# Optimization experiments

Hardware: AMD Instinct MI355X
Metric: run time of the kernel (lower is better)

Reference implementation:

```python
import jax, jax.numpy as jnp
import numpy as np

B, S, D, F, E, K = 2, 2048, 1024, 4096, 8, 2


def setup_inputs() -> dict:
    key = jax.random.key(0)
    ks = jax.random.split(key, 6)
    s = 0.02  # init scale
    return {
        "x": jax.random.normal(ks[0], (B, S, D), dtype=jnp.float32),
        "Wr": jax.random.normal(ks[1], (D, E), dtype=jnp.float32) * s,
        "br": jnp.zeros((E,), dtype=jnp.float32),
        "W1": jax.random.normal(ks[2], (E, D, F), dtype=jnp.float32) * s,
        "b1": jnp.zeros((E, F), dtype=jnp.float32),
        "W2": jax.random.normal(ks[3], (E, F, D), dtype=jnp.float32) * s,
        "b2": jnp.zeros((E, D), dtype=jnp.float32),
        "top_k": K,
    }


def reference(x, Wr, br, W1, b1, W2, b2, top_k):
    b, s, d = x.shape
    e = Wr.shape[1]
    xt = x.reshape(-1, d)                              # [T, D], T = b*s
    logits = xt @ Wr + br                              # [T, E]
    probs = jax.nn.softmax(logits, axis=-1)            # [T, E] router probabilities
    topw, topi = jax.lax.top_k(probs, top_k)           # [T, K] each
    # combine weight per (token, expert): weight if expert in token's top-k else 0
    cw = jnp.sum(jax.nn.one_hot(topi, e, dtype=x.dtype) * topw[..., None], axis=1)  # [T, E]
    # dense grouped FFN: every expert over every token, then weighted combine
    h = jax.nn.relu(jnp.einsum('td,edf->tef', xt, W1) + b1)   # [T, E, F]
    y = jnp.einsum('tef,efd->ted', h, W2) + b2                # [T, E, D]
    out = jnp.einsum('te,ted->td', cw, y).reshape(b, s, d)    # [B, S, D]
    return out, probs.reshape(b, s, e)
```

## Files before the change

kernel.cpp:

```cpp
#include <hip/hip_runtime.h>
#include <hip/hip_bf16.h>


#define T_TOK 4096
#define D_DIM 1024
#define F_DIM 4096
#define E_NUM 8
#define CAP_ROWS 9216
#define N_TILES (CAP_ROWS/128)

typedef __attribute__((ext_vector_type(8))) short short8v;
typedef __attribute__((ext_vector_type(8))) unsigned short ushort8v;
typedef __attribute__((ext_vector_type(4))) float f32x4;

static __device__ __forceinline__ unsigned short f2bf(float f){
  union { float f; unsigned u; } v; v.f = f;
  unsigned r = (v.u + 0x7fffu + ((v.u >> 16) & 1u)) >> 16;
  return (unsigned short)r;
}
static __device__ __forceinline__ float bf2f(unsigned short s){
  union { unsigned u; float f; } v; v.u = ((unsigned)s) << 16;
  return v.f;
}

static __device__ __forceinline__ void gload16(const void* g, void* l) {
  __builtin_amdgcn_global_load_lds(
      (const __attribute__((address_space(1))) unsigned int*)g,
      (__attribute__((address_space(3))) unsigned int*)l, 16, 0, 0);
}

__global__ __launch_bounds__(256) void k_init(int* counts, int* cursor,
                                              int* rows_token, float* rows_w){
  const int gid = blockIdx.x * 256 + threadIdx.x;
  if (gid < E_NUM) counts[gid] = 0;
  else if (gid < 2*E_NUM) cursor[gid - E_NUM] = 0;
  if (gid < CAP_ROWS) { rows_token[gid] = 0; rows_w[gid] = 0.f; }
}

__global__ __launch_bounds__(256) void k_router(
    const float* __restrict__ x, const float* __restrict__ Wr,
    const float* __restrict__ br, float* __restrict__ probs_out,
    int* __restrict__ topi, float* __restrict__ topw, int* __restrict__ counts,
    unsigned short* __restrict__ xbf)
{
  const int lane = threadIdx.x & 63;
  const int t = blockIdx.x * 4 + (threadIdx.x >> 6);
  float xv[16];
  #pragma unroll
  for (int i = 0; i < 16; ++i) xv[i] = x[(size_t)t*D_DIM + i*64 + lane];
  #pragma unroll
  for (int i = 0; i < 16; ++i) xbf[(size_t)t*D_DIM + i*64 + lane] = f2bf(xv[i]);
  float pe[E_NUM];
  #pragma unroll
  for (int e = 0; e < E_NUM; ++e) {
    float p = 0.f;
    #pragma unroll
    for (int i = 0; i < 16; ++i) p += xv[i] * Wr[(i*64 + lane)*E_NUM + e];
    #pragma unroll
    for (int off = 32; off >= 1; off >>= 1) p += __shfl_xor(p, off);
    pe[e] = p + br[e];
  }
  float m = pe[0];
  #pragma unroll
  for (int e = 1; e < E_NUM; ++e) m = fmaxf(m, pe[e]);
  float s = 0.f;
  #pragma unroll
  for (int e = 0; e < E_NUM; ++e) { pe[e] = expf(pe[e] - m); s += pe[e]; }
  const float inv = 1.f / s;
  int e1 = 0; float v1 = pe[0];
  #pragma unroll
  for (int e = 1; e < E_NUM; ++e) if (pe[e] > v1) { v1 = pe[e]; e1 = e; }
  int e2 = (e1 == 0) ? 1 : 0; float v2 = pe[e2];
  #pragma unroll
  for (int e = 0; e < E_NUM; ++e) if (e != e1 && pe[e] > v2) { v2 = pe[e]; e2 = e; }
  if (lane == 0) {
    #pragma unroll
    for (int e = 0; e < E_NUM; ++e) probs_out[(size_t)t*E_NUM + e] = pe[e] * inv;
    topi[t*2+0] = e1; topw[t*2+0] = v1 * inv;
    topi[t*2+1] = e2; topw[t*2+1] = v2 * inv;
    atomicAdd(&counts[e1], 1);
    atomicAdd(&counts[e2], 1);
  }
}

__global__ __launch_bounds__(256) void k_scan(
    const int* __restrict__ counts, int* __restrict__ pbase,
    int* __restrict__ tile_e)
{
  __shared__ int base_s[E_NUM + 1];
  const int tid = threadIdx.x;
  if (tid == 0) {
    int base = 0;
    #pragma unroll
    for (int e = 0; e < E_NUM; ++e) {
      base_s[e] = base;
      base += ((counts[e] + 127) >> 7) << 7;
    }
    base_s[E_NUM] = base;
  }
  __syncthreads();
  if (tid <= E_NUM) pbase[tid] = base_s[tid];
  if (tid < N_TILES) {
    const int r0 = tid << 7;
    int e = -1;
    #pragma unroll
    for (int k = 0; k < E_NUM; ++k)
      if (r0 >= base_s[k] && r0 < base_s[k+1]) e = k;
    tile_e[tid] = e;
  }
}

__global__ __launch_bounds__(256) void k_assign(
    const int* __restrict__ topi, const float* __restrict__ topw,
    const int* __restrict__ pbase, int* __restrict__ cursor,
    int* __restrict__ rows_token, float* __restrict__ rows_w,
    int* __restrict__ pair_of)
{
  const int t = blockIdx.x * 256 + threadIdx.x;
  if (t < T_TOK) {
    #pragma unroll
    for (int k = 0; k < 2; ++k) {
      const int e = topi[t*2+k];
      const int slot = atomicAdd(&cursor[e], 1);
      const int pid = pbase[e] + slot;
      rows_token[pid] = t;
      rows_w[pid] = topw[t*2+k];
      pair_of[t*2+k] = pid;
    }
  }
}

template<int R, int C>
__global__ __launch_bounds__(256) void k_tcvt(const float* __restrict__ in,
                                              unsigned short* __restrict__ out)
{
  const size_t eo = (size_t)blockIdx.z * R * C;
  const int r0 = blockIdx.y * 64, c0 = blockIdx.x * 64;
  __shared__ unsigned short ls[64][66];
  const int t = threadIdx.x;
  const int rr = t >> 4, cc = (t & 15) * 4;
  #pragma unroll
  for (int p = 0; p < 4; ++p) {
    const float4 v = *(const float4*)&in[eo + (size_t)(r0 + p*16 + rr)*C + c0 + cc];
    ls[p*16+rr][cc+0]=f2bf(v.x); ls[p*16+rr][cc+1]=f2bf(v.y);
    ls[p*16+rr][cc+2]=f2bf(v.z); ls[p*16+rr][cc+3]=f2bf(v.w);
  }
  __syncthreads();
  const int kc = (t & 7) * 8, nn0 = t >> 3;
  #pragma unroll
  for (int p = 0; p < 2; ++p) {
    const int nn = nn0 + p*32;
    ushort8v o;
    #pragma unroll
    for (int j = 0; j < 8; ++j) o[j] = ls[kc + j][nn];
    *(ushort8v*)&out[eo + (size_t)(c0 + nn)*R + r0 + kc] = o;
  }
}

template<bool GATHER, int NDIM, int KDIM, bool EPI1>
__global__ __launch_bounds__(256, 2) void k_gemm(
    const unsigned short* __restrict__ A,
    const unsigned short* __restrict__ Bt,
    const float* __restrict__ bias,
    const int* __restrict__ tile_e,
    const int* __restrict__ rows_token,
    const float* __restrict__ rows_w,
    unsigned short* __restrict__ outp)
{
  const int tot = gridDim.x * gridDim.y;
  int flat = blockIdx.x * gridDim.y + blockIdx.y;
  flat = (flat & 7) * (tot >> 3) + (flat >> 3);
  const int bx = flat / gridDim.y;
  const int by = flat % gridDim.y;
  const int e = tile_e[by];
  if (e < 0) return;
  const int rt = by * 128;
  const int ntc = bx * 128;
  __shared__ __align__(16) unsigned short LB[3][2][128*32];
  const int tid = threadIdx.x;
  const int lane = tid & 63;
  const int w = tid >> 6;
  const int seg = w & 1;
  const int isB = (w >= 2) ? 1 : 0;
  const int lrow = lane >> 2, lchunk = lane & 3;
  const unsigned short* gsrc[4];
  unsigned lds_off[4];
  if (w < 2) {
    #pragma unroll
    for (int i = 0; i < 4; ++i) {
      const int rl = seg*64 + i*16 + lrow;
      const int rowidx = GATHER ? rows_token[rt + rl] : (rt + rl);
      gsrc[i] = A + (size_t)rowidx * KDIM + lchunk*8;
      lds_off[i] = (unsigned)((seg*64 + i*16)*32);
    }
  } else {
    const unsigned short* Be = Bt + (size_t)e * NDIM * KDIM;
    #pragma unroll
    for (int i = 0; i < 4; ++i) {
      const int rl = seg*64 + i*16 + lrow;
      gsrc[i] = Be + (size_t)(ntc + rl) * KDIM + lchunk*8;
      lds_off[i] = (unsigned)((seg*64 + i*16)*32);
    }
  }
  const int wr = w >> 1, wc = w & 1;
  const int cl = lane & 15, rgb = lane >> 4;
  f32x4 acc[4][4] = {};

  constexpr int NT = KDIM / 32;
  #pragma unroll
  for (int i = 0; i < 4; ++i) gload16(gsrc[i] + 0,  &LB[0][isB][lds_off[i]]);
  #pragma unroll
  for (int i = 0; i < 4; ++i) gload16(gsrc[i] + 32, &LB[1][isB][lds_off[i]]);
  asm volatile("s_waitcnt vmcnt(4)" ::: "memory");
  __builtin_amdgcn_s_barrier();

  int buf = 0;
  for (int t = 0; t < NT; ++t) {
    const int pb = (buf == 0) ? 2 : (buf - 1);
    if (t + 2 < NT) {
      const int kof = (t + 2) * 32;
      #pragma unroll
      for (int i = 0; i < 4; ++i) gload16(gsrc[i] + kof, &LB[pb][isB][lds_off[i]]);
    }
    short8v a[4], b[4];
    #pragma unroll
    for (int m = 0; m < 4; ++m)
      a[m] = *(const short8v*)&LB[buf][0][(wr*64 + m*16 + cl)*32 + rgb*8];
    #pragma unroll
    for (int n = 0; n < 4; ++n)
      b[n] = *(const short8v*)&LB[buf][1][(wc*64 + n*16 + cl)*32 + rgb*8];
    #pragma unroll
    for (int m = 0; m < 4; ++m)
      #pragma unroll
      for (int n = 0; n < 4; ++n)
        acc[m][n] = __builtin_amdgcn_mfma_f32_16x16x32_bf16(a[m], b[n], acc[m][n], 0, 0, 0);
    if (t + 2 < NT) {
      asm volatile("s_waitcnt vmcnt(4)" ::: "memory");
    } else {
      asm volatile("s_waitcnt vmcnt(0)" ::: "memory");
    }
    __builtin_amdgcn_s_barrier();
    buf = (buf == 2) ? 0 : (buf + 1);
  }

  const size_t ebias = (size_t)e * NDIM;
  #pragma unroll
  for (int n = 0; n < 4; ++n) {
    const int col = ntc + wc*64 + n*16 + cl;
    const float bv = bias[ebias + col];
    #pragma unroll
    for (int m = 0; m < 4; ++m) {
      const int row = rt + wr*64 + m*16 + rgb*4;
      #pragma unroll
      for (int r = 0; r < 4; ++r) {
        float v = acc[m][n][r] + bv;
        if (EPI1) v = fmaxf(v, 0.f);
        else      v *= rows_w[row + r];
        const unsigned short hb = f2bf(v);
        const unsigned short ob = (unsigned short)__shfl_xor((int)(unsigned)hb, 1);
        if ((lane & 1) == 0) {
          const unsigned pk = (unsigned)hb | ((unsigned)ob << 16);
          *(unsigned*)&outp[(size_t)(row + r)*NDIM + col] = pk;
        }
      }
    }
  }
}

__global__ __launch_bounds__(256) void k_combine(
    const unsigned short* __restrict__ y, const int* __restrict__ pair_of,
    float* __restrict__ out)
{
  const int gid = blockIdx.x * 256 + threadIdx.x;
  const int t = gid >> 7;
  const int c = (gid & 127) * 8;
  const int p0 = pair_of[t*2+0];
  const int p1 = pair_of[t*2+1];
  const ushort8v a = *(const ushort8v*)&y[(size_t)p0*D_DIM + c];
  const ushort8v b = *(const ushort8v*)&y[(size_t)p1*D_DIM + c];
  float o[8];
  #pragma unroll
  for (int j = 0; j < 8; ++j) o[j] = bf2f(a[j]) + bf2f(b[j]);
  float4 o0; o0.x=o[0]; o0.y=o[1]; o0.z=o[2]; o0.w=o[3];
  float4 o1; o1.x=o[4]; o1.y=o[5]; o1.z=o[6]; o1.w=o[7];
  *(float4*)&out[(size_t)t*D_DIM + c]     = o0;
  *(float4*)&out[(size_t)t*D_DIM + c + 4] = o1;
}

extern "C" void kernel_launch(void* const* d_in, const int* in_sizes, int n_in,
                              void* d_out, int out_size, void* d_ws, size_t ws_size,
                              hipStream_t stream)
{
  const float* x  = (const float*)d_in[0];
  const float* Wr = (const float*)d_in[1];
  const float* br = (const float*)d_in[2];
  const float* W1 = (const float*)d_in[3];
  const float* b1 = (const float*)d_in[4];
  const float* W2 = (const float*)d_in[5];
  const float* b2 = (const float*)d_in[6];
  (void)in_sizes; (void)n_in; (void)out_size; (void)ws_size;

  float* out   = (float*)d_out;
  float* probs = out + (size_t)T_TOK * D_DIM;

  char* w = (char*)d_ws;
  size_t off = 0;
  int*   counts     = (int*)(w + off); off += 256;
  int*   cursor     = (int*)(w + off); off += 256;
  int*   pbase      = (int*)(w + off); off += 512;
  int*   tile_e     = (int*)(w + off); off += 3072;
  int*   topi       = (int*)(w + off); off += (size_t)T_TOK*2*4;
  float* topw       = (float*)(w + off); off += (size_t)T_TOK*2*4;
  int*   pair_of    = (int*)(w + off); off += (size_t)T_TOK*2*4;
  int*   rows_token = (int*)(w + off); off += (size_t)CAP_ROWS*4;
  float* rows_w     = (float*)(w + off); off += (size_t)CAP_ROWS*4;
  off = (off + 255) & ~(size_t)255;
  unsigned short* xbf = (unsigned short*)(w + off); off += (size_t)T_TOK*D_DIM*2;
  unsigned short* Wt  = (unsigned short*)(w + off); off += (size_t)E_NUM*D_DIM*F_DIM*2;
  unsigned short* h   = (unsigned short*)(w + off); off += (size_t)CAP_ROWS*F_DIM*2;
  unsigned short* y   = (unsigned short*)(w + off); off += (size_t)CAP_ROWS*D_DIM*2;

  k_init<<<(CAP_ROWS + 255) / 256, 256, 0, stream>>>(counts, cursor, rows_token, rows_w);
  k_router<<<T_TOK / 4, 256, 0, stream>>>(x, Wr, br, probs, topi, topw, counts, xbf);
  k_scan<<<1, 256, 0, stream>>>(counts, pbase, tile_e);
  k_assign<<<T_TOK / 256, 256, 0, stream>>>(topi, topw, pbase, cursor,
                                            rows_token, rows_w, pair_of);
  k_tcvt<D_DIM, F_DIM><<<dim3(F_DIM/64, D_DIM/64, E_NUM), 256, 0, stream>>>(W1, Wt);
  k_gemm<true, F_DIM, D_DIM, true><<<dim3(F_DIM/128, N_TILES), 256, 0, stream>>>(
      xbf, Wt, b1, tile_e, rows_token, rows_w, h);
  k_tcvt<F_DIM, D_DIM><<<dim3(D_DIM/64, F_DIM/64, E_NUM), 256, 0, stream>>>(W2, Wt);
  k_gemm<false, D_DIM, F_DIM, false><<<dim3(D_DIM/128, N_TILES), 256, 0, stream>>>(
      h, Wt, b2, tile_e, rows_token, rows_w, y);
  k_combine<<<T_TOK * D_DIM / 8 / 256, 256, 0, stream>>>(y, pair_of, out);
}
```

Baseline: 475.2 us.

## Enlarge GEMM tiles to 256x128 with K=64 stages, swizzled LDS and 8 waves

Reworks the grouped expert GEMM to use 256-row by 128-column tiles with 512 threads. Each pipeline stage now covers 64 of K, stored in XOR-swizzled LDS to avoid bank conflicts. The inner loop is split into two halves that interleave the next stage's global-to-LDS loads with MFMA bursts, and raises wave priority around the MFMAs. Expert row padding goes to multiples of 256, which enlarges capacity and adds padded work per expert. The weight transpose kernel now keeps fp32 in LDS and converts to bf16 on the output side.

```diff
diff --git a/kernel.cpp b/kernel.cpp
--- a/kernel.cpp
+++ b/kernel.cpp
@@ -6,8 +6,8 @@
 #define D_DIM 1024
 #define F_DIM 4096
 #define E_NUM 8
-#define CAP_ROWS 9216
-#define N_TILES (CAP_ROWS/128)
+#define CAP_ROWS 10240
+#define N_TILES (CAP_ROWS/256)
 
 typedef __attribute__((ext_vector_type(8))) short short8v;
 typedef __attribute__((ext_vector_type(8))) unsigned short ushort8v;
@@ -94,14 +94,14 @@
     #pragma unroll
     for (int e = 0; e < E_NUM; ++e) {
       base_s[e] = base;
-      base += ((counts[e] + 127) >> 7) << 7;
+      base += ((counts[e] + 255) >> 8) << 8;
     }
     base_s[E_NUM] = base;
   }
   __syncthreads();
   if (tid <= E_NUM) pbase[tid] = base_s[tid];
   if (tid < N_TILES) {
-    const int r0 = tid << 7;
+    const int r0 = tid << 8;
     int e = -1;
     #pragma unroll
     for (int k = 0; k < E_NUM; ++k)
@@ -136,29 +136,28 @@
 {
   const size_t eo = (size_t)blockIdx.z * R * C;
   const int r0 = blockIdx.y * 64, c0 = blockIdx.x * 64;
-  __shared__ unsigned short ls[64][66];
+  __shared__ float ls[64][67];
   const int t = threadIdx.x;
   const int rr = t >> 4, cc = (t & 15) * 4;
   #pragma unroll
   for (int p = 0; p < 4; ++p) {
     const float4 v = *(const float4*)&in[eo + (size_t)(r0 + p*16 + rr)*C + c0 + cc];
-    ls[p*16+rr][cc+0]=f2bf(v.x); ls[p*16+rr][cc+1]=f2bf(v.y);
-    ls[p*16+rr][cc+2]=f2bf(v.z); ls[p*16+rr][cc+3]=f2bf(v.w);
+    ls[p*16+rr][cc+0]=v.x; ls[p*16+rr][cc+1]=v.y;
+    ls[p*16+rr][cc+2]=v.z; ls[p*16+rr][cc+3]=v.w;
   }
   __syncthreads();
-  const int kc = (t & 7) * 8, nn0 = t >> 3;
-  #pragma unroll
-  for (int p = 0; p < 2; ++p) {
-    const int nn = nn0 + p*32;
-    ushort8v o;
-    #pragma unroll
-    for (int j = 0; j < 8; ++j) o[j] = ls[kc + j][nn];
-    *(ushort8v*)&out[eo + (size_t)(c0 + nn)*R + r0 + kc] = o;
-  }
-}
-
-template<bool GATHER, int NDIM, int KDIM, bool EPI1>
-__global__ __launch_bounds__(256, 2) void k_gemm(
+  const int nn = t >> 2, seg = (t & 3) * 16;
+  ushort8v o0, o1;
+  #pragma unroll
+  for (int j = 0; j < 8; ++j) o0[j] = f2bf(ls[seg + j][nn]);
+  #pragma unroll
+  for (int j = 0; j < 8; ++j) o1[j] = f2bf(ls[seg + 8 + j][nn]);
+  *(ushort8v*)&out[eo + (size_t)(c0 + nn)*R + r0 + seg]     = o0;
+  *(ushort8v*)&out[eo + (size_t)(c0 + nn)*R + r0 + seg + 8] = o1;
+}
+
+template<bool GATHER, int NDIM, int NKT, int EPI>
+__global__ __launch_bounds__(512) void k_gemm(
     const unsigned short* __restrict__ A,
     const unsigned short* __restrict__ Bt,
     const float* __restrict__ bias,
@@ -167,6 +166,7 @@
     const float* __restrict__ rows_w,
     unsigned short* __restrict__ outp)
 {
+  constexpr int KDIM = NKT * 64;
   const int tot = gridDim.x * gridDim.y;
   int flat = blockIdx.x * gridDim.y + blockIdx.y;
   flat = (flat & 7) * (tot >> 3) + (flat >> 3);
@@ -174,74 +174,102 @@
   const int by = flat % gridDim.y;
   const int e = tile_e[by];
   if (e < 0) return;
-  const int rt = by * 128;
+  const int rt = by * 256;
   const int ntc = bx * 128;
-  __shared__ __align__(16) unsigned short LB[3][2][128*32];
+  __shared__ __align__(16) unsigned short LB[3][384 * 64];
   const int tid = threadIdx.x;
   const int lane = tid & 63;
   const int w = tid >> 6;
-  const int seg = w & 1;
-  const int isB = (w >= 2) ? 1 : 0;
-  const int lrow = lane >> 2, lchunk = lane & 3;
-  const unsigned short* gsrc[4];
-  unsigned lds_off[4];
-  if (w < 2) {
-    #pragma unroll
-    for (int i = 0; i < 4; ++i) {
-      const int rl = seg*64 + i*16 + lrow;
-      const int rowidx = GATHER ? rows_token[rt + rl] : (rt + rl);
-      gsrc[i] = A + (size_t)rowidx * KDIM + lchunk*8;
-      lds_off[i] = (unsigned)((seg*64 + i*16)*32);
-    }
-  } else {
+  const int trow = tid >> 3;
+  const int g = (tid & 7) ^ (trow & 7);
+  const unsigned short* gp[6];
+  unsigned lbase[6];
+  #pragma unroll
+  for (int c = 0; c < 4; ++c) {
+    const int rl = c*64 + trow;
+    const int rowidx = GATHER ? rows_token[rt + rl] : (rt + rl);
+    gp[c] = A + (size_t)rowidx * KDIM + g*8;
+    lbase[c] = (unsigned)((c*64 + w*8) * 64);
+  }
+  {
     const unsigned short* Be = Bt + (size_t)e * NDIM * KDIM;
     #pragma unroll
-    for (int i = 0; i < 4; ++i) {
-      const int rl = seg*64 + i*16 + lrow;
-      gsrc[i] = Be + (size_t)(ntc + rl) * KDIM + lchunk*8;
-      lds_off[i] = (unsigned)((seg*64 + i*16)*32);
+    for (int c = 4; c < 6; ++c) {
+      const int rl = (c-4)*64 + trow;
+      gp[c] = Be + (size_t)(ntc + rl) * KDIM + g*8;
+      lbase[c] = (unsigned)((256 + (c-4)*64 + w*8) * 64);
     }
   }
   const int wr = w >> 1, wc = w & 1;
   const int cl = lane & 15, rgb = lane >> 4;
+  const int swz = cl & 7;
   f32x4 acc[4][4] = {};
 
-  constexpr int NT = KDIM / 32;
-  #pragma unroll
-  for (int i = 0; i < 4; ++i) gload16(gsrc[i] + 0,  &LB[0][isB][lds_off[i]]);
-  #pragma unroll
-  for (int i = 0; i < 4; ++i) gload16(gsrc[i] + 32, &LB[1][isB][lds_off[i]]);
-  asm volatile("s_waitcnt vmcnt(4)" ::: "memory");
+  #define STAGE3(tt, c0_)                                            \
+    { const int _s = (tt) % 3; const size_t _ko = (size_t)(tt) * 64; \
+      gload16(gp[c0_+0] + _ko, &LB[_s][lbase[c0_+0]]);               \
+      gload16(gp[c0_+1] + _ko, &LB[_s][lbase[c0_+1]]);               \
+      gload16(gp[c0_+2] + _ko, &LB[_s][lbase[c0_+2]]); }
+
+  STAGE3(0, 0) STAGE3(0, 3)
+  STAGE3(1, 0) STAGE3(1, 3)
+  asm volatile("s_waitcnt vmcnt(6)" ::: "memory");
   __builtin_amdgcn_s_barrier();
 
-  int buf = 0;
-  for (int t = 0; t < NT; ++t) {
-    const int pb = (buf == 0) ? 2 : (buf - 1);
-    if (t + 2 < NT) {
-      const int kof = (t + 2) * 32;
-      #pragma unroll
-      for (int i = 0; i < 4; ++i) gload16(gsrc[i] + kof, &LB[pb][isB][lds_off[i]]);
-    }
-    short8v a[4], b[4];
-    #pragma unroll
-    for (int m = 0; m < 4; ++m)
-      a[m] = *(const short8v*)&LB[buf][0][(wr*64 + m*16 + cl)*32 + rgb*8];
-    #pragma unroll
-    for (int n = 0; n < 4; ++n)
-      b[n] = *(const short8v*)&LB[buf][1][(wc*64 + n*16 + cl)*32 + rgb*8];
-    #pragma unroll
-    for (int m = 0; m < 4; ++m)
+  for (int t = 0; t < NKT; ++t) {
+    const unsigned short* Sb = LB[t % 3];
+    short8v b[4][2];
+    {
+      short8v a[2][2];
+      #pragma unroll
+      for (int m = 0; m < 2; ++m)
+        #pragma unroll
+        for (int ks = 0; ks < 2; ++ks)
+          a[m][ks] = *(const short8v*)&Sb[(wr*64 + m*16 + cl)*64 + ((ks*4+rgb)^swz)*8];
       #pragma unroll
       for (int n = 0; n < 4; ++n)
-        acc[m][n] = __builtin_amdgcn_mfma_f32_16x16x32_bf16(a[m], b[n], acc[m][n], 0, 0, 0);
-    if (t + 2 < NT) {
-      asm volatile("s_waitcnt vmcnt(4)" ::: "memory");
-    } else {
-      asm volatile("s_waitcnt vmcnt(0)" ::: "memory");
-    }
-    __builtin_amdgcn_s_barrier();
-    buf = (buf == 2) ? 0 : (buf + 1);
-  }
+        #pragma unroll
+        for (int ks = 0; ks < 2; ++ks)
+          b[n][ks] = *(const short8v*)&Sb[(256 + wc*64 + n*16 + cl)*64 + ((ks*4+rgb)^swz)*8];
+      if (t + 2 < NKT) STAGE3(t+2, 0)
+      __builtin_amdgcn_s_barrier();
+      __builtin_amdgcn_s_setprio(1);
+      #pragma unroll
+      for (int m = 0; m < 2; ++m)
+        #pragma unroll
+        for (int n = 0; n < 4; ++n)
+          #pragma unroll
+          for (int ks = 0; ks < 2; ++ks)
+            acc[m][n] = __builtin_amdgcn_mfma_f32_16x16x32_bf16(a[m][ks], b[n][ks], acc[m][n], 0, 0, 0);
+      __builtin_amdgcn_s_setprio(0);
+      __builtin_amdgcn_s_barrier();
+    }
+    {
+      short8v a[2][2];
+      #pragma unroll
+      for (int m = 0; m < 2; ++m)
+        #pragma unroll
+        for (int ks = 0; ks < 2; ++ks)
+          a[m][ks] = *(const short8v*)&Sb[(wr*64 + (m+2)*16 + cl)*64 + ((ks*4+rgb)^swz)*8];
+      if (t + 2 < NKT) STAGE3(t+2, 3)
+      __builtin_amdgcn_s_barrier();
+      __builtin_amdgcn_s_setprio(1);
+      #pragma unroll
+      for (int m = 0; m < 2; ++m)
+        #pragma unroll
+        for (int n = 0; n < 4; ++n)
+          #pragma unroll
+          for (int ks = 0; ks < 2; ++ks)
+            acc[m+2][n] = __builtin_amdgcn_mfma_f32_16x16x32_bf16(a[m][ks], b[n][ks], acc[m+2][n], 0, 0, 0);
+      __builtin_amdgcn_s_setprio(0);
+      if (t + 1 < NKT) {
+        if (t + 2 < NKT) { asm volatile("s_waitcnt vmcnt(6)" ::: "memory"); }
+        else             { asm volatile("s_waitcnt vmcnt(0)" ::: "memory"); }
+        __builtin_amdgcn_s_barrier();
+      }
+    }
+  }
+  #undef STAGE3
 
   const size_t ebias = (size_t)e * NDIM;
   #pragma unroll
@@ -254,8 +282,8 @@
       #pragma unroll
       for (int r = 0; r < 4; ++r) {
         float v = acc[m][n][r] + bv;
-        if (EPI1) v = fmaxf(v, 0.f);
-        else      v *= rows_w[row + r];
+        if (EPI == 1) v = fmaxf(v, 0.f);
+        else          v *= rows_w[row + r];
         const unsigned short hb = f2bf(v);
         const unsigned short ob = (unsigned short)__shfl_xor((int)(unsigned)hb, 1);
         if ((lane & 1) == 0) {
@@ -326,10 +354,10 @@
   k_assign<<<T_TOK / 256, 256, 0, stream>>>(topi, topw, pbase, cursor,
                                             rows_token, rows_w, pair_of);
   k_tcvt<D_DIM, F_DIM><<<dim3(F_DIM/64, D_DIM/64, E_NUM), 256, 0, stream>>>(W1, Wt);
-  k_gemm<true, F_DIM, D_DIM, true><<<dim3(F_DIM/128, N_TILES), 256, 0, stream>>>(
+  k_gemm<true, F_DIM, 16, 1><<<dim3(F_DIM/128, N_TILES), 512, 0, stream>>>(
       xbf, Wt, b1, tile_e, rows_token, rows_w, h);
   k_tcvt<F_DIM, D_DIM><<<dim3(D_DIM/64, F_DIM/64, E_NUM), 256, 0, stream>>>(W2, Wt);
-  k_gemm<false, D_DIM, F_DIM, false><<<dim3(D_DIM/128, N_TILES), 256, 0, stream>>>(
+  k_gemm<false, D_DIM, 64, 2><<<dim3(D_DIM/128, N_TILES), 512, 0, stream>>>(
       h, Wt, b2, tile_e, rows_token, rows_w, y);
   k_combine<<<T_TOK * D_DIM / 8 / 256, 256, 0, stream>>>(y, pair_of, out);
 }
```

Result: faster. 456.8 us (-3.9%).

## Use 256x256 GEMM tiles with 512 threads, swizzled LDS and split-K for down-proj

Applied to the files above, without the earlier changes.

Enlarges the grouped GEMM block tile from 128x128 to 256x256 with eight waves, padding expert segments to 256 rows. LDS chunk addressing is XOR-swizzled to cut bank conflicts. The second GEMM is split along K into up to four partial outputs, sized by available workspace, and the combine kernel sums them. This raises operand reuse and keeps the down-projection grid large enough to fill the device. The cost is extra padded rows, larger partial-output traffic, and bf16 rounding on each partial sum.

```diff
diff --git a/kernel.cpp b/kernel.cpp
--- a/kernel.cpp
+++ b/kernel.cpp
@@ -6,8 +6,8 @@
 #define D_DIM 1024
 #define F_DIM 4096
 #define E_NUM 8
-#define CAP_ROWS 9216
-#define N_TILES (CAP_ROWS/128)
+#define CAP_ROWS 10240
+#define N_TILES (CAP_ROWS/256)
 
 typedef __attribute__((ext_vector_type(8))) short short8v;
 typedef __attribute__((ext_vector_type(8))) unsigned short ushort8v;
@@ -94,14 +94,14 @@
     #pragma unroll
     for (int e = 0; e < E_NUM; ++e) {
       base_s[e] = base;
-      base += ((counts[e] + 127) >> 7) << 7;
+      base += ((counts[e] + 255) >> 8) << 8;
     }
     base_s[E_NUM] = base;
   }
   __syncthreads();
   if (tid <= E_NUM) pbase[tid] = base_s[tid];
   if (tid < N_TILES) {
-    const int r0 = tid << 7;
+    const int r0 = tid << 8;
     int e = -1;
     #pragma unroll
     for (int k = 0; k < E_NUM; ++k)
@@ -157,15 +157,16 @@
   }
 }
 
-template<bool GATHER, int NDIM, int KDIM, bool EPI1>
-__global__ __launch_bounds__(256, 2) void k_gemm(
+template<bool GATHER, int NDIM, int KFULL, int EPI>
+__global__ __launch_bounds__(512, 2) void k_gemm(
     const unsigned short* __restrict__ A,
     const unsigned short* __restrict__ Bt,
     const float* __restrict__ bias,
     const int* __restrict__ tile_e,
     const int* __restrict__ rows_token,
     const float* __restrict__ rows_w,
-    unsigned short* __restrict__ outp)
+    unsigned short* __restrict__ outp,
+    int nkt, int kch)
 {
   const int tot = gridDim.x * gridDim.y;
   int flat = blockIdx.x * gridDim.y + blockIdx.y;
@@ -174,93 +175,98 @@
   const int by = flat % gridDim.y;
   const int e = tile_e[by];
   if (e < 0) return;
-  const int rt = by * 128;
-  const int ntc = bx * 128;
-  __shared__ __align__(16) unsigned short LB[3][2][128*32];
+  const int rt = by * 256;
+  const int ntc = bx * 256;
+  const int koff = blockIdx.z * kch;
+  __shared__ __align__(16) unsigned short LB[3][512*32];
   const int tid = threadIdx.x;
   const int lane = tid & 63;
   const int w = tid >> 6;
-  const int seg = w & 1;
-  const int isB = (w >= 2) ? 1 : 0;
-  const int lrow = lane >> 2, lchunk = lane & 3;
-  const unsigned short* gsrc[4];
-  unsigned lds_off[4];
-  if (w < 2) {
+  const int lrow = lane >> 2;
+  const int g = (lane & 3) ^ (lrow & 3);
+  const unsigned short* gp[4];
+  unsigned lbase[4];
+  if (w < 4) {
     #pragma unroll
     for (int i = 0; i < 4; ++i) {
-      const int rl = seg*64 + i*16 + lrow;
+      const int rl = w*64 + i*16 + lrow;
       const int rowidx = GATHER ? rows_token[rt + rl] : (rt + rl);
-      gsrc[i] = A + (size_t)rowidx * KDIM + lchunk*8;
-      lds_off[i] = (unsigned)((seg*64 + i*16)*32);
+      gp[i] = A + (size_t)rowidx * KFULL + koff + g*8;
+      lbase[i] = (unsigned)((w*64 + i*16) * 32);
     }
   } else {
-    const unsigned short* Be = Bt + (size_t)e * NDIM * KDIM;
+    const unsigned short* Be = Bt + (size_t)e * NDIM * KFULL;
     #pragma unroll
     for (int i = 0; i < 4; ++i) {
-      const int rl = seg*64 + i*16 + lrow;
-      gsrc[i] = Be + (size_t)(ntc + rl) * KDIM + lchunk*8;
-      lds_off[i] = (unsigned)((seg*64 + i*16)*32);
-    }
-  }
-  const int wr = w >> 1, wc = w & 1;
+      const int rl = (w-4)*64 + i*16 + lrow;
+      gp[i] = Be + (size_t)(ntc + rl) * KFULL + koff + g*8;
+      lbase[i] = (unsigned)((256 + (w-4)*64 + i*16) * 32);
+    }
+  }
+  const int wr = w >> 2, wc = w & 3;
   const int cl = lane & 15, rgb = lane >> 4;
-  f32x4 acc[4][4] = {};
-
-  constexpr int NT = KDIM / 32;
-  #pragma unroll
-  for (int i = 0; i < 4; ++i) gload16(gsrc[i] + 0,  &LB[0][isB][lds_off[i]]);
-  #pragma unroll
-  for (int i = 0; i < 4; ++i) gload16(gsrc[i] + 32, &LB[1][isB][lds_off[i]]);
+  const int ch = (rgb ^ (cl & 3)) * 8;
+  f32x4 acc[8][4] = {};
+
+  #define STG(tt, ss)                                  \
+    { const int _ko = (tt) * 32;                       \
+      gload16(gp[0] + _ko, &LB[ss][lbase[0]]);         \
+      gload16(gp[1] + _ko, &LB[ss][lbase[1]]);         \
+      gload16(gp[2] + _ko, &LB[ss][lbase[2]]);         \
+      gload16(gp[3] + _ko, &LB[ss][lbase[3]]); }
+
+  STG(0, 0)
+  STG(1, 1)
   asm volatile("s_waitcnt vmcnt(4)" ::: "memory");
   __builtin_amdgcn_s_barrier();
 
-  int buf = 0;
-  for (int t = 0; t < NT; ++t) {
-    const int pb = (buf == 0) ? 2 : (buf - 1);
-    if (t + 2 < NT) {
-      const int kof = (t + 2) * 32;
-      #pragma unroll
-      for (int i = 0; i < 4; ++i) gload16(gsrc[i] + kof, &LB[pb][isB][lds_off[i]]);
-    }
-    short8v a[4], b[4];
-    #pragma unroll
-    for (int m = 0; m < 4; ++m)
-      a[m] = *(const short8v*)&LB[buf][0][(wr*64 + m*16 + cl)*32 + rgb*8];
+  int cur = 0;
+  for (int t = 0; t < nkt; ++t) {
+    const int pb = (cur == 0) ? 2 : (cur - 1);
+    if (t + 2 < nkt) STG(t+2, pb)
+    const unsigned short* Sb = LB[cur];
+    short8v a[8], b[4];
+    #pragma unroll
+    for (int m = 0; m < 8; ++m)
+      a[m] = *(const short8v*)&Sb[(wr*128 + m*16 + cl)*32 + ch];
     #pragma unroll
     for (int n = 0; n < 4; ++n)
-      b[n] = *(const short8v*)&LB[buf][1][(wc*64 + n*16 + cl)*32 + rgb*8];
-    #pragma unroll
-    for (int m = 0; m < 4; ++m)
+      b[n] = *(const short8v*)&Sb[(256 + wc*64 + n*16 + cl)*32 + ch];
+    #pragma unroll
+    for (int m = 0; m < 8; ++m)
       #pragma unroll
       for (int n = 0; n < 4; ++n)
         acc[m][n] = __builtin_amdgcn_mfma_f32_16x16x32_bf16(a[m], b[n], acc[m][n], 0, 0, 0);
-    if (t + 2 < NT) {
-      asm volatile("s_waitcnt vmcnt(4)" ::: "memory");
-    } else {
-      asm volatile("s_waitcnt vmcnt(0)" ::: "memory");
-    }
+    if (t + 2 < nkt) { asm volatile("s_waitcnt vmcnt(4)" ::: "memory"); }
+    else             { asm volatile("s_waitcnt vmcnt(0)" ::: "memory"); }
     __builtin_amdgcn_s_barrier();
-    buf = (buf == 2) ? 0 : (buf + 1);
-  }
-
+    cur = (cur == 2) ? 0 : (cur + 1);
+  }
+  #undef STG
+
+  unsigned short* op = outp;
+  if (EPI == 2) op += (size_t)blockIdx.z * CAP_ROWS * NDIM;
+  const bool addb = (EPI == 1) || (blockIdx.z == 0);
   const size_t ebias = (size_t)e * NDIM;
   #pragma unroll
-  for (int n = 0; n < 4; ++n) {
-    const int col = ntc + wc*64 + n*16 + cl;
-    const float bv = bias[ebias + col];
-    #pragma unroll
-    for (int m = 0; m < 4; ++m) {
-      const int row = rt + wr*64 + m*16 + rgb*4;
+  for (int m = 0; m < 8; ++m) {
+    const int row = rt + wr*128 + m*16 + rgb*4;
+    float4 rw4 = make_float4(0,0,0,0);
+    if (EPI == 2) rw4 = *(const float4*)&rows_w[row];
+    #pragma unroll
+    for (int n = 0; n < 4; ++n) {
+      const int col = ntc + wc*64 + n*16 + cl;
+      const float bv = addb ? bias[ebias + col] : 0.f;
       #pragma unroll
       for (int r = 0; r < 4; ++r) {
         float v = acc[m][n][r] + bv;
-        if (EPI1) v = fmaxf(v, 0.f);
-        else      v *= rows_w[row + r];
+        if (EPI == 1) v = fmaxf(v, 0.f);
+        else          v *= ((const float*)&rw4)[r];
         const unsigned short hb = f2bf(v);
         const unsigned short ob = (unsigned short)__shfl_xor((int)(unsigned)hb, 1);
         if ((lane & 1) == 0) {
           const unsigned pk = (unsigned)hb | ((unsigned)ob << 16);
-          *(unsigned*)&outp[(size_t)(row + r)*NDIM + col] = pk;
+          *(unsigned*)&op[(size_t)(row + r)*NDIM + col] = pk;
         }
       }
     }
@@ -268,19 +274,22 @@
 }
 
 __global__ __launch_bounds__(256) void k_combine(
-    const unsigned short* __restrict__ y, const int* __restrict__ pair_of,
-    float* __restrict__ out)
+    const unsigned short* __restrict__ yp, const int* __restrict__ pair_of,
+    float* __restrict__ out, int ksplit)
 {
   const int gid = blockIdx.x * 256 + threadIdx.x;
   const int t = gid >> 7;
   const int c = (gid & 127) * 8;
-  const int p0 = pair_of[t*2+0];
-  const int p1 = pair_of[t*2+1];
-  const ushort8v a = *(const ushort8v*)&y[(size_t)p0*D_DIM + c];
-  const ushort8v b = *(const ushort8v*)&y[(size_t)p1*D_DIM + c];
-  float o[8];
-  #pragma unroll
-  for (int j = 0; j < 8; ++j) o[j] = bf2f(a[j]) + bf2f(b[j]);
+  float o[8] = {0,0,0,0,0,0,0,0};
+  #pragma unroll
+  for (int k = 0; k < 2; ++k) {
+    const int p = pair_of[t*2+k];
+    for (int s = 0; s < ksplit; ++s) {
+      const ushort8v v = *(const ushort8v*)&yp[((size_t)s*CAP_ROWS + p)*D_DIM + c];
+      #pragma unroll
+      for (int j = 0; j < 8; ++j) o[j] += bf2f(v[j]);
+    }
+  }
   float4 o0; o0.x=o[0]; o0.y=o[1]; o0.z=o[2]; o0.w=o[3];
   float4 o1; o1.x=o[4]; o1.y=o[5]; o1.z=o[6]; o1.w=o[7];
   *(float4*)&out[(size_t)t*D_DIM + c]     = o0;
@@ -298,7 +307,7 @@
   const float* b1 = (const float*)d_in[4];
   const float* W2 = (const float*)d_in[5];
   const float* b2 = (const float*)d_in[6];
-  (void)in_sizes; (void)n_in; (void)out_size; (void)ws_size;
+  (void)in_sizes; (void)n_in; (void)out_size;
 
   float* out   = (float*)d_out;
   float* probs = out + (size_t)T_TOK * D_DIM;
@@ -318,7 +327,13 @@
   unsigned short* xbf = (unsigned short*)(w + off); off += (size_t)T_TOK*D_DIM*2;
   unsigned short* Wt  = (unsigned short*)(w + off); off += (size_t)E_NUM*D_DIM*F_DIM*2;
   unsigned short* h   = (unsigned short*)(w + off); off += (size_t)CAP_ROWS*F_DIM*2;
-  unsigned short* y   = (unsigned short*)(w + off); off += (size_t)CAP_ROWS*D_DIM*2;
+  unsigned short* yp  = (unsigned short*)(w + off);
+  const size_t ypart_bytes = (size_t)CAP_ROWS * D_DIM * 2;
+  int ksplit = 1;
+  if (ws_size >= off + 4 * ypart_bytes) ksplit = 4;
+  else if (ws_size >= off + 2 * ypart_bytes) ksplit = 2;
+  const int kch2 = F_DIM / ksplit;
+  const int nkt2 = kch2 / 32;
 
   k_init<<<(CAP_ROWS + 255) / 256, 256, 0, stream>>>(counts, cursor, rows_token, rows_w);
   k_router<<<T_TOK / 4, 256, 0, stream>>>(x, Wr, br, probs, topi, topw, counts, xbf);
@@ -326,10 +341,10 @@
   k_assign<<<T_TOK / 256, 256, 0, stream>>>(topi, topw, pbase, cursor,
                                             rows_token, rows_w, pair_of);
   k_tcvt<D_DIM, F_DIM><<<dim3(F_DIM/64, D_DIM/64, E_NUM), 256, 0, stream>>>(W1, Wt);
-  k_gemm<true, F_DIM, D_DIM, true><<<dim3(F_DIM/128, N_TILES), 256, 0, stream>>>(
-      xbf, Wt, b1, tile_e, rows_token, rows_w, h);
+  k_gemm<true, F_DIM, D_DIM, 1><<<dim3(F_DIM/256, N_TILES, 1), 512, 0, stream>>>(
+      xbf, Wt, b1, tile_e, rows_token, rows_w, h, D_DIM/32, D_DIM);
   k_tcvt<F_DIM, D_DIM><<<dim3(D_DIM/64, F_DIM/64, E_NUM), 256, 0, stream>>>(W2, Wt);
-  k_gemm<false, D_DIM, F_DIM, false><<<dim3(D_DIM/128, N_TILES), 256, 0, stream>>>(
-      h, Wt, b2, tile_e, rows_token, rows_w, y);
-  k_combine<<<T_TOK * D_DIM / 8 / 256, 256, 0, stream>>>(y, pair_of, out);
-}
+  k_gemm<false, D_DIM, F_DIM, 2><<<dim3(D_DIM/256, N_TILES, ksplit), 512, 0, stream>>>(
+      h, Wt, b2, tile_e, rows_token, rows_w, yp, nkt2, kch2);
+  k_combine<<<T_TOK * D_DIM / 8 / 256, 256, 0, stream>>>(yp, pair_of, out, ksplit);
+}
```

After: 475.1 us. About the same (-0.0%).
